# Optimization experiments

Measured on AMD Instinct MI355X. Metric: run time of the kernel, lower is better.

The kernel has to match this reference:

```python
import jax, jax.numpy as jnp
import numpy as np

GAMMA = 1.0
INF_REPLACE = 1e10  # original code replaces inf with 1e10 before logsumexp


def _softmin3(r_diag, r_up, r_left, gamma):
    # softmin over the 3 DP neighbors (stack order matches original: diag, up, left)
    x = jnp.stack([r_diag, r_up, r_left], axis=0)  # (3, B)
    x = jnp.where(jnp.isinf(x), jnp.asarray(INF_REPLACE, x.dtype), x)
    return -gamma * jax.nn.logsumexp(-x / gamma, axis=0)  # (B,)


def _cdist(X, Y):
    # Euclidean pairwise distance, torch.cdist(p=2): (B,N,d),(B,M,d) -> (B,N,M)
    d2 = (jnp.sum(X * X, axis=-1)[:, :, None]
          + jnp.sum(Y * Y, axis=-1)[:, None, :]
          - 2.0 * jnp.einsum('bnd,bmd->bnm', X, Y))
    return jnp.sqrt(jnp.maximum(d2, 0.0))


def _soft_dtw(X, Y, gamma):
    B, N, _ = X.shape
    D = _cdist(X, Y)  # (B, N, N)
    inf = jnp.asarray(jnp.inf, D.dtype)

    # R row 0: [0, inf, inf, ...] per batch
    prev_row0 = jnp.full((B, N + 1), inf, dtype=D.dtype).at[:, 0].set(0.0)

    def row_step(prev_row, d_row):
        # prev_row: (B, N+1) = R[i-1, :]; d_row: (B, N) = D[:, i-1, :]
        xs = (d_row.T, prev_row[:, :-1].T, prev_row[:, 1:].T)  # each (N, B)

        def col_step(r_left, x):
            d, r_diag, r_up = x  # each (B,)
            r = d + _softmin3(r_diag, r_up, r_left, gamma)
            return r, r

        _, row = jax.lax.scan(col_step, jnp.full((B,), inf, dtype=D.dtype), xs)
        new_row = jnp.concatenate([jnp.full((B, 1), inf, dtype=D.dtype), row.T], axis=1)
        return new_row, None

    last_row, _ = jax.lax.scan(row_step, prev_row0, jnp.swapaxes(D, 0, 1))
    return last_row[:, -1]  # R[:, N, N], shape (B,)


def setup_inputs() -> dict:
    key = jax.random.key(0)
    kx, ky = jax.random.split(key)
    B, N, d = 64, 512, 64
    X = jax.random.normal(kx, (B, N, d), dtype=jnp.float32)
    Y = jax.random.normal(ky, (B, N, d), dtype=jnp.float32)
    return {"X": X, "Y": Y}


def reference(X, Y):
    return _soft_dtw(X, Y, GAMMA)
```

## Files before the change

kernel.cpp:

```cpp
#include <hip/hip_runtime.h>
#include <math.h>

#define NB 64
#define NN 512
#define ND 64

#define LOG2E 1.4426950408889634f
#define LN2   0.6931471805599453f
#define RING  12
#define NINF  __int_as_float(0xFF800000u)

typedef __attribute__((ext_vector_type(8))) short  bf16x8;
typedef __attribute__((ext_vector_type(4))) float  f32x4;

static __device__ __forceinline__ unsigned short f2bf(float f) {
    unsigned u = __float_as_uint(f);
    u += 0x7FFFu + ((u >> 16) & 1u);
    return (unsigned short)(u >> 16);
}

__global__ __launch_bounds__(256) void pack_kernel(const float* __restrict__ X,
                                                   const float* __restrict__ Y,
                                                   unsigned short* __restrict__ Xp,
                                                   unsigned short* __restrict__ Yp,
                                                   float* __restrict__ nx,
                                                   float* __restrict__ ny) {
    const int gid = blockIdx.x * 256 + threadIdx.x;
    const float* src;
    unsigned short* dst;
    float* ndst;
    if (blockIdx.y == 0) { src = X + (size_t)gid * ND; dst = Xp; ndst = nx; }
    else                 { src = Y + (size_t)gid * ND; dst = Yp; ndst = ny; }

    float v[ND];
    float s = 0.f;
    #pragma unroll
    for (int k = 0; k < ND; k += 4) {
        float4 f = *(const float4*)(src + k);
        v[k] = f.x; v[k + 1] = f.y; v[k + 2] = f.z; v[k + 3] = f.w;
        s += f.x * f.x + f.y * f.y + f.z * f.z + f.w * f.w;
    }
    ndst[gid] = s;

    const int b  = gid >> 9;
    const int i  = gid & 511;
    const int it = i >> 4;
    const int lm = i & 15;
    #pragma unroll
    for (int h = 0; h < 2; ++h) {
        #pragma unroll
        for (int q = 0; q < 4; ++q) {
            unsigned w[4];
            #pragma unroll
            for (int m = 0; m < 4; ++m) {
                const int c = h * 32 + q * 8 + 2 * m;
                w[m] = (unsigned)f2bf(v[c]) | ((unsigned)f2bf(v[c + 1]) << 16);
            }
            uint4 pkt; pkt.x = w[0]; pkt.y = w[1]; pkt.z = w[2]; pkt.w = w[3];
            *(uint4*)(dst + ((((size_t)b * 32 + it) * 2 + h) << 9)
                          + (size_t)(q * 16 + lm) * 8) = pkt;
        }
    }
}

__global__ __launch_bounds__(256) void cdist_kernel(const unsigned short* __restrict__ Xp,
                                                    const unsigned short* __restrict__ Yp,
                                                    const float* __restrict__ nx,
                                                    const float* __restrict__ ny,
                                                    unsigned short* __restrict__ Wt) {
    const int b  = blockIdx.z;
    const int ib = blockIdx.x * 128;
    const int jb = blockIdx.y * 128;
    const int t  = threadIdx.x;

    const int wave = t >> 6;
    const int wi   = (wave & 1) * 64;
    const int wj   = (wave >> 1) * 64;
    const int lane = t & 63;
    const int lm   = lane & 15;
    const int quad = lane >> 4;

    f32x4 acc[4][4];
    #pragma unroll
    for (int mt = 0; mt < 4; ++mt)
        #pragma unroll
        for (int nt = 0; nt < 4; ++nt)
            acc[mt][nt] = (f32x4){0.f, 0.f, 0.f, 0.f};

    const int jt0 = (jb + wj) >> 4;
    const int it0 = (ib + wi) >> 4;

    #pragma unroll
    for (int h = 0; h < 2; ++h) {
        bf16x8 Af[4], Bf[4];
        #pragma unroll
        for (int mt = 0; mt < 4; ++mt)
            Af[mt] = *(const bf16x8*)(Yp
                + ((((size_t)b * 32 + jt0 + mt) * 2 + h) << 9) + (size_t)lane * 8);
        #pragma unroll
        for (int nt = 0; nt < 4; ++nt)
            Bf[nt] = *(const bf16x8*)(Xp
                + ((((size_t)b * 32 + it0 + nt) * 2 + h) << 9) + (size_t)lane * 8);
        #pragma unroll
        for (int mt = 0; mt < 4; ++mt)
            #pragma unroll
            for (int nt = 0; nt < 4; ++nt)
                acc[mt][nt] = __builtin_amdgcn_mfma_f32_16x16x32_bf16(
                    Af[mt], Bf[nt], acc[mt][nt], 0, 0, 0);
    }

    float nxv[4];
    float4 nyv[4];
    #pragma unroll
    for (int nt = 0; nt < 4; ++nt)
        nxv[nt] = nx[(size_t)b * NN + ib + wi + nt * 16 + lm];
    #pragma unroll
    for (int mt = 0; mt < 4; ++mt)
        nyv[mt] = *(const float4*)(ny + (size_t)b * NN + jb + wj + mt * 16 + quad * 4);

    #pragma unroll
    for (int nt = 0; nt < 4; ++nt) {
        const int i = ib + wi + nt * 16 + lm;
        unsigned short* Drow = Wt + ((size_t)b * NN + i) * NN + jb + wj;
        #pragma unroll
        for (int mt = 0; mt < 4; ++mt) {
            const float* nyp = (const float*)&nyv[mt];
            unsigned a[4];
            #pragma unroll
            for (int r = 0; r < 4; ++r) {
                float d2 = nyp[r] + nxv[nt] - 2.0f * acc[mt][nt][r];
                float w  = __builtin_amdgcn_exp2f(16.0f - LOG2E * sqrtf(fmaxf(d2, 0.f)));
                a[r] = __float_as_uint(w) + 0x8000u;
            }
            uint2 pkt;
            pkt.x = (a[0] >> 16) | (a[1] & 0xFFFF0000u);
            pkt.y = (a[2] >> 16) | (a[3] & 0xFFFF0000u);
            *(uint2*)(Drow + mt * 16 + quad * 4) = pkt;
        }
    }
}

static __device__ __forceinline__ void dtw_step(
    bool DOACT, bool DOGUARD, bool DOREN, bool DOCLAMP,
    int ss, int u, int t, const unsigned short* __restrict__ Wb, int ib,
    uint4* ring, float* L, float& diagHold, float& h, float& Otf)
{
    const float recvH = __int_as_float(__builtin_amdgcn_update_dpp(
        (int)0xFF800000, __float_as_int(h), 0x138 , 0xf, 0xf, false));

    if (DOACT) { if (ss == t && t > 0) Otf = -recvH; }

    const float up0   = __builtin_amdgcn_exp2f(fminf(recvH + Otf, 80.0f));
    const float diag0 = diagHold;
    diagHold = up0 * 65536.0f;

    const int j = ss - t + 1;
    const uint4 c = ring[u];

    {
        int jn = j + RING;
        if (DOCLAMP) jn = jn < 1 ? 1 : jn;
        ring[u] = *(const uint4*)(Wb + (size_t)(jn - 1) * NN + ib);
    }

    bool act = true;
    if (DOGUARD) act = (j >= 1) && (j <= NN);
    if (act) {
        float dd[8];
        dd[0] = __uint_as_float(c.x << 16);
        dd[1] = __uint_as_float(c.x & 0xFFFF0000u);
        dd[2] = __uint_as_float(c.y << 16);
        dd[3] = __uint_as_float(c.y & 0xFFFF0000u);
        dd[4] = __uint_as_float(c.z << 16);
        dd[5] = __uint_as_float(c.z & 0xFFFF0000u);
        dd[6] = __uint_as_float(c.w << 16);
        dd[7] = __uint_as_float(c.w & 0xFFFF0000u);

        float pre[8], cc[8];
        pre[0] = diag0 + L[0];
        #pragma unroll
        for (int k = 1; k < 8; ++k)
            pre[k] = fmaf(65536.0f, L[k - 1], L[k]);
        #pragma unroll
        for (int k = 0; k < 8; ++k) cc[k] = dd[k] * pre[k];
        float r = up0;
        #pragma unroll
        for (int k = 0; k < 8; ++k) {
            r = fmaf(dd[k], r, cc[k]);
            L[k] = r;
        }

        if (DOREN) {
            float m8 = fmaxf(fmaxf(fmaxf(L[0], L[1]), fmaxf(L[2], L[3])),
                             fmaxf(fmaxf(L[4], L[5]), fmaxf(L[6], L[7])));
            const int   e  = (int)(__float_as_uint(m8) >> 23) - 127;
            const float sc = __uint_as_float((unsigned)(127 - e) << 23);
            #pragma unroll
            for (int k = 0; k < 8; ++k) L[k] *= sc;
            diagHold *= sc;
            Otf -= (float)e;
        }

        h = __builtin_amdgcn_logf(L[7]) - Otf;
    }
}

__global__ __launch_bounds__(64) void dtw_kernel(const unsigned short* __restrict__ Wt,
                                                 float* __restrict__ out) {
    const int b = blockIdx.x;
    const int t = threadIdx.x;
    const unsigned short* __restrict__ Wb = Wt + (size_t)b * NN * NN;
    const int ib = 8 * t;

    float L[8];
    #pragma unroll
    for (int k = 0; k < 8; ++k) L[k] = 0.0f;

    float diagHold = (t == 0) ? 65536.0f : 0.0f;
    float h        = NINF;
    float Otf      = 0.0f;

    uint4 ring[RING];
    #pragma unroll
    for (int u = 0; u < RING; ++u) {
        int col = u - t + 1;
        col = col < 1 ? 1 : col;
        ring[u] = *(const uint4*)(Wb + (size_t)(col - 1) * NN + ib);
    }

    for (int sb = 0; sb < 72; sb += RING)
        #pragma unroll
        for (int u = 0; u < RING; ++u)
            dtw_step(true, true, (u & 1) == 1, true,
                     sb + u, u, t, Wb, ib, ring, L, diagHold, h, Otf);

    for (int sb = 72; sb < 504; sb += RING)
        #pragma unroll
        for (int u = 0; u < RING; ++u)
            dtw_step(false, false, (u & 1) == 1, false,
                     sb + u, u, t, Wb, ib, ring, L, diagHold, h, Otf);

    for (int sb = 504; sb < 576; sb += RING)
        #pragma unroll
        for (int u = 0; u < RING; ++u)
            dtw_step(false, true, (u & 1) == 1, false,
                     sb + u, u, t, Wb, ib, ring, L, diagHold, h, Otf);

    if (t == 63) out[b] = (16384.0f - h) * LN2;
}

extern "C" void kernel_launch(void* const* d_in, const int* in_sizes, int n_in,
                              void* d_out, int out_size, void* d_ws, size_t ws_size,
                              hipStream_t stream) {
    const float* X = (const float*)d_in[0];
    const float* Y = (const float*)d_in[1];
    float* out = (float*)d_out;

    char* ws = (char*)d_ws;
    unsigned short* Wt = (unsigned short*)(ws);
    unsigned short* Xp = (unsigned short*)(ws + (33554432));
    unsigned short* Yp = (unsigned short*)(ws + (33554432 + 4194304));
    float* nx = (float*)(ws + (33554432 + 2 * 4194304));
    float* ny = (float*)(ws + (33554432 + 2 * 4194304 + 131072));

    pack_kernel<<<dim3(NB * NN / 256, 2), 256, 0, stream>>>(X, Y, Xp, Yp, nx, ny);
    cdist_kernel<<<dim3(4, 4, NB), 256, 0, stream>>>(Xp, Yp, nx, ny, Wt);
    dtw_kernel<<<NB, 64, 0, stream>>>(Wt, out);
}
```

Baseline: 153.4 us.

## Split soft-DTW wavefront across two waves with LDS handoff of boundary rows

The DTW kernel now uses two 64-lane waves per batch, each owning 256 rows with 4 rows per lane instead of 8, so the serial dependency chain per step is halved. Wave 1 runs two chunks behind wave 0 and receives wave 0's last-row values through shared memory, exchanged once per 64-step chunk with a block barrier and shifted across lanes via DPP. The ring prefetch depth grows to 16 with narrower loads. The cost is roughly 128 extra steps of pipeline fill, eleven block barriers, and LDS traffic, while the number of waves per CU doubles.

New measurement: 147.3 us. 1.04x faster.

```diff
diff --git a/kernel.cpp b/kernel.cpp
--- a/kernel.cpp
+++ b/kernel.cpp
@@ -7,7 +7,7 @@
 
 #define LOG2E 1.4426950408889634f
 #define LN2   0.6931471805599453f
-#define RING  12
+#define RING  16
 #define NINF  __int_as_float(0xFF800000u)
 
 typedef __attribute__((ext_vector_type(8))) short  bf16x8;
@@ -140,113 +140,138 @@
     }
 }
 
-static __device__ __forceinline__ void dtw_step(
-    bool DOACT, bool DOGUARD, bool DOREN, bool DOCLAMP,
+static __device__ __forceinline__ float dpp_shr1(float x, float old) {
+    return __int_as_float(__builtin_amdgcn_update_dpp(
+        __float_as_int(old), __float_as_int(x), 0x138, 0xf, 0xf, false));
+}
+static __device__ __forceinline__ float dpp_shl1(float x) {
+    return __int_as_float(__builtin_amdgcn_update_dpp(
+        0, __float_as_int(x), 0x130, 0xf, 0xf, false));
+}
+
+static __device__ __forceinline__ void dtw_step4(
+    bool W1, bool DOACT, bool DOGUARD, bool DOCLAMP, bool DOREN,
     int ss, int u, int t, const unsigned short* __restrict__ Wb, int ib,
-    uint4* ring, float* L, float& diagHold, float& h, float& Otf)
+    uint2* ring, float* L, float& diagHold, float& h, float& Otf,
+    float& hbuf, float* __restrict__ h0)
 {
-    const float recvH = __int_as_float(__builtin_amdgcn_update_dpp(
-        (int)0xFF800000, __float_as_int(h), 0x138 , 0xf, 0xf, false));
-
-    if (DOACT) { if (ss == t && t > 0) Otf = -recvH; }
+    float recvH = dpp_shr1(h, NINF);
+    if (W1) {
+        recvH = (t == 0) ? hbuf : recvH;
+        hbuf  = dpp_shl1(hbuf);
+    }
+    if (DOACT) { if (ss == t && (t > 0 || W1)) Otf = -recvH; }
 
     const float up0   = __builtin_amdgcn_exp2f(fminf(recvH + Otf, 80.0f));
     const float diag0 = diagHold;
     diagHold = up0 * 65536.0f;
 
     const int j = ss - t + 1;
-    const uint4 c = ring[u];
+    const uint2 c = ring[u];
 
     {
         int jn = j + RING;
         if (DOCLAMP) jn = jn < 1 ? 1 : jn;
-        ring[u] = *(const uint4*)(Wb + (size_t)(jn - 1) * NN + ib);
+        ring[u] = *(const uint2*)(Wb + (size_t)(jn - 1) * NN + ib);
     }
 
     bool act = true;
     if (DOGUARD) act = (j >= 1) && (j <= NN);
     if (act) {
-        float dd[8];
+        float dd[4];
         dd[0] = __uint_as_float(c.x << 16);
         dd[1] = __uint_as_float(c.x & 0xFFFF0000u);
         dd[2] = __uint_as_float(c.y << 16);
         dd[3] = __uint_as_float(c.y & 0xFFFF0000u);
-        dd[4] = __uint_as_float(c.z << 16);
-        dd[5] = __uint_as_float(c.z & 0xFFFF0000u);
-        dd[6] = __uint_as_float(c.w << 16);
-        dd[7] = __uint_as_float(c.w & 0xFFFF0000u);
-
-        float pre[8], cc[8];
+
+        float pre[4], cc[4];
         pre[0] = diag0 + L[0];
         #pragma unroll
-        for (int k = 1; k < 8; ++k)
+        for (int k = 1; k < 4; ++k)
             pre[k] = fmaf(65536.0f, L[k - 1], L[k]);
         #pragma unroll
-        for (int k = 0; k < 8; ++k) cc[k] = dd[k] * pre[k];
+        for (int k = 0; k < 4; ++k) cc[k] = dd[k] * pre[k];
         float r = up0;
         #pragma unroll
-        for (int k = 0; k < 8; ++k) {
+        for (int k = 0; k < 4; ++k) {
             r = fmaf(dd[k], r, cc[k]);
             L[k] = r;
         }
 
         if (DOREN) {
-            float m8 = fmaxf(fmaxf(fmaxf(L[0], L[1]), fmaxf(L[2], L[3])),
-                             fmaxf(fmaxf(L[4], L[5]), fmaxf(L[6], L[7])));
-            const int   e  = (int)(__float_as_uint(m8) >> 23) - 127;
+            float m4 = fmaxf(fmaxf(L[0], L[1]), fmaxf(L[2], L[3]));
+            const int   e  = (int)(__float_as_uint(m4) >> 23) - 127;
             const float sc = __uint_as_float((unsigned)(127 - e) << 23);
             #pragma unroll
-            for (int k = 0; k < 8; ++k) L[k] *= sc;
+            for (int k = 0; k < 4; ++k) L[k] *= sc;
             diagHold *= sc;
             Otf -= (float)e;
         }
 
-        h = __builtin_amdgcn_logf(L[7]) - Otf;
-    }
-}
-
-__global__ __launch_bounds__(64) void dtw_kernel(const unsigned short* __restrict__ Wt,
-                                                 float* __restrict__ out) {
-    const int b = blockIdx.x;
-    const int t = threadIdx.x;
+        h = __builtin_amdgcn_logf(L[3]) - Otf;
+        if (!W1) h0[j] = h;
+    }
+}
+
+static __device__ __forceinline__ void run_chunk(
+    bool W1, bool ACT, bool GUARD, bool CLAMP, int base,
+    int t, const unsigned short* __restrict__ Wb, int ib,
+    uint2* ring, float* L, float& diagHold, float& h, float& Otf,
+    float& hbuf, float* __restrict__ h0)
+{
+    for (int sb = 0; sb < 64; sb += RING)
+        #pragma unroll
+        for (int u = 0; u < RING; ++u)
+            dtw_step4(W1, ACT, GUARD, CLAMP, (u & 1) == 1,
+                      base + sb + u, u, t, Wb, ib, ring, L,
+                      diagHold, h, Otf, hbuf, h0);
+}
+
+__global__ __launch_bounds__(128) void dtw_kernel(const unsigned short* __restrict__ Wt,
+                                                  float* __restrict__ out) {
+    __shared__ float h0[584];
+    const int b    = blockIdx.x;
+    const int tid  = threadIdx.x;
+    const int t    = tid & 63;
+    const int wave = tid >> 6;
     const unsigned short* __restrict__ Wb = Wt + (size_t)b * NN * NN;
-    const int ib = 8 * t;
-
-    float L[8];
-    #pragma unroll
-    for (int k = 0; k < 8; ++k) L[k] = 0.0f;
-
-    float diagHold = (t == 0) ? 65536.0f : 0.0f;
-    float h        = NINF;
-    float Otf      = 0.0f;
-
-    uint4 ring[RING];
+    const int ib = wave * 256 + 4 * t;
+
+    float L[4] = {0.f, 0.f, 0.f, 0.f};
+    float diagHold = (wave == 0 && t == 0) ? 65536.0f : 0.0f;
+    float h = NINF, Otf = 0.0f, hbuf = NINF;
+
+    uint2 ring[RING];
     #pragma unroll
     for (int u = 0; u < RING; ++u) {
         int col = u - t + 1;
         col = col < 1 ? 1 : col;
-        ring[u] = *(const uint4*)(Wb + (size_t)(col - 1) * NN + ib);
-    }
-
-    for (int sb = 0; sb < 72; sb += RING)
-        #pragma unroll
-        for (int u = 0; u < RING; ++u)
-            dtw_step(true, true, (u & 1) == 1, true,
-                     sb + u, u, t, Wb, ib, ring, L, diagHold, h, Otf);
-
-    for (int sb = 72; sb < 504; sb += RING)
-        #pragma unroll
-        for (int u = 0; u < RING; ++u)
-            dtw_step(false, false, (u & 1) == 1, false,
-                     sb + u, u, t, Wb, ib, ring, L, diagHold, h, Otf);
-
-    for (int sb = 504; sb < 576; sb += RING)
-        #pragma unroll
-        for (int u = 0; u < RING; ++u)
-            dtw_step(false, true, (u & 1) == 1, false,
-                     sb + u, u, t, Wb, ib, ring, L, diagHold, h, Otf);
-
-    if (t == 63) out[b] = (16384.0f - h) * LN2;
+        ring[u] = *(const uint2*)(Wb + (size_t)(col - 1) * NN + ib);
+    }
+
+    for (int wall = 0; wall < 11; ++wall) {
+        const int ch = wave ? wall - 2 : wall;
+        if (wave == 0) {
+            if (ch == 0)
+                run_chunk(false, true,  true,  true,  0,      t, Wb, ib, ring, L, diagHold, h, Otf, hbuf, h0);
+            else if (ch >= 1 && ch <= 7)
+                run_chunk(false, false, false, false, ch*64,  t, Wb, ib, ring, L, diagHold, h, Otf, hbuf, h0);
+            else if (ch == 8)
+                run_chunk(false, false, true,  false, 512,    t, Wb, ib, ring, L, diagHold, h, Otf, hbuf, h0);
+        } else {
+            if (ch == 0)
+                run_chunk(true,  true,  true,  true,  0,      t, Wb, ib, ring, L, diagHold, h, Otf, hbuf, h0);
+            else if (ch >= 1 && ch <= 7)
+                run_chunk(true,  false, false, false, ch*64,  t, Wb, ib, ring, L, diagHold, h, Otf, hbuf, h0);
+            else if (ch == 8)
+                run_chunk(true,  false, true,  false, 512,    t, Wb, ib, ring, L, diagHold, h, Otf, hbuf, h0);
+        }
+        __syncthreads();
+        if (wave && wall >= 1 && wall <= 9)
+            hbuf = h0[(wall - 1) * 64 + 1 + t];
+    }
+
+    if (wave == 1 && t == 63) out[b] = (16384.0f - h) * LN2;
 }
 
 extern "C" void kernel_launch(void* const* d_in, const int* in_sizes, int n_in,
@@ -265,5 +290,5 @@
 
     pack_kernel<<<dim3(NB * NN / 256, 2), 256, 0, stream>>>(X, Y, Xp, Yp, nx, ny);
     cdist_kernel<<<dim3(4, 4, NB), 256, 0, stream>>>(Xp, Yp, nx, ny, Wt);
-    dtw_kernel<<<NB, 64, 0, stream>>>(Wt, out);
-}
+    dtw_kernel<<<NB, 128, 0, stream>>>(Wt, out);
+}
```

## Interleave two batch DTW chains per wavefront and pass log as mantissa/exponent

Applied to the files above, without the earlier changes.

Each DTW block now processes two batch items with interleaved independent recurrences, launching half as many blocks, so the latency of one serial chain can be hidden by the other. The log/exp2 pair on the critical path is replaced by passing the neighbor value as a mantissa plus an integer exponent and rebuilding it with integer exponent arithmetic. The prefetch ring shrinks from 12 to 8 entries per chain to limit register pressure. The trade-off is fewer wavefronts across the GPU (32 instead of 64), higher register use per thread, and a shorter prefetch distance.

Measured after the change: 219.4 us. 43.1% more time.

```diff
diff --git a/kernel.cpp b/kernel.cpp
--- a/kernel.cpp
+++ b/kernel.cpp
@@ -7,8 +7,7 @@
 
 #define LOG2E 1.4426950408889634f
 #define LN2   0.6931471805599453f
-#define RING  12
-#define NINF  __int_as_float(0xFF800000u)
+#define RING  8
 
 typedef __attribute__((ext_vector_type(8))) short  bf16x8;
 typedef __attribute__((ext_vector_type(4))) float  f32x4;
@@ -140,19 +139,36 @@
     }
 }
 
-static __device__ __forceinline__ void dtw_step(
-    bool DOACT, bool DOGUARD, bool DOREN, bool DOCLAMP,
+static __device__ __forceinline__ float dpp_shr1f(float x, float old) {
+    return __int_as_float(__builtin_amdgcn_update_dpp(
+        __float_as_int(old), __float_as_int(x), 0x138, 0xf, 0xf, false));
+}
+static __device__ __forceinline__ int dpp_shr1i(int x, int old) {
+    return __builtin_amdgcn_update_dpp(old, x, 0x138, 0xf, 0xf, false);
+}
+
+struct DtwState {
+    float L[8];
+    float diagHold;
+    float hm;
+    int   he;
+    int   Oti;
+};
+
+static __device__ __forceinline__ void half_step(
+    bool DOACT, bool DOGUARD, bool DOCLAMP, bool DOREN,
     int ss, int u, int t, const unsigned short* __restrict__ Wb, int ib,
-    uint4* ring, float* L, float& diagHold, float& h, float& Otf)
+    uint4* ring, DtwState& S)
 {
-    const float recvH = __int_as_float(__builtin_amdgcn_update_dpp(
-        (int)0xFF800000, __float_as_int(h), 0x138 , 0xf, 0xf, false));
-
-    if (DOACT) { if (ss == t && t > 0) Otf = -recvH; }
-
-    const float up0   = __builtin_amdgcn_exp2f(fminf(recvH + Otf, 80.0f));
-    const float diag0 = diagHold;
-    diagHold = up0 * 65536.0f;
+    const float rm = dpp_shr1f(S.hm, 1.0f);
+    const int   re = dpp_shr1i(S.he, -100000);
+    if (DOACT) { if (ss == t && t > 0) S.Oti = -re; }
+
+    int sx = re + S.Oti;
+    sx = sx < -126 ? -126 : (sx > 60 ? 60 : sx);
+    const float up0 = __uint_as_float(__float_as_uint(rm) + ((unsigned)sx << 23));
+    const float diag0 = S.diagHold;
+    S.diagHold = up0 * 65536.0f;
 
     const int j = ss - t + 1;
     const uint4 c = ring[u];
@@ -177,76 +193,87 @@
         dd[7] = __uint_as_float(c.w & 0xFFFF0000u);
 
         float pre[8], cc[8];
-        pre[0] = diag0 + L[0];
+        pre[0] = diag0 + S.L[0];
         #pragma unroll
         for (int k = 1; k < 8; ++k)
-            pre[k] = fmaf(65536.0f, L[k - 1], L[k]);
+            pre[k] = fmaf(65536.0f, S.L[k - 1], S.L[k]);
         #pragma unroll
         for (int k = 0; k < 8; ++k) cc[k] = dd[k] * pre[k];
         float r = up0;
         #pragma unroll
         for (int k = 0; k < 8; ++k) {
             r = fmaf(dd[k], r, cc[k]);
-            L[k] = r;
+            S.L[k] = r;
         }
 
         if (DOREN) {
-            float m8 = fmaxf(fmaxf(fmaxf(L[0], L[1]), fmaxf(L[2], L[3])),
-                             fmaxf(fmaxf(L[4], L[5]), fmaxf(L[6], L[7])));
+            float m8 = fmaxf(fmaxf(fmaxf(S.L[0], S.L[1]), fmaxf(S.L[2], S.L[3])),
+                             fmaxf(fmaxf(S.L[4], S.L[5]), fmaxf(S.L[6], S.L[7])));
             const int   e  = (int)(__float_as_uint(m8) >> 23) - 127;
             const float sc = __uint_as_float((unsigned)(127 - e) << 23);
             #pragma unroll
-            for (int k = 0; k < 8; ++k) L[k] *= sc;
-            diagHold *= sc;
-            Otf -= (float)e;
-        }
-
-        h = __builtin_amdgcn_logf(L[7]) - Otf;
+            for (int k = 0; k < 8; ++k) S.L[k] *= sc;
+            S.diagHold *= sc;
+            S.Oti -= e;
+        }
+
+        const unsigned lb = __float_as_uint(S.L[7]);
+        S.he = (int)(lb >> 23) - 127 - S.Oti;
+        S.hm = __uint_as_float((lb & 0x007FFFFFu) | 0x3F800000u);
     }
 }
 
 __global__ __launch_bounds__(64) void dtw_kernel(const unsigned short* __restrict__ Wt,
                                                  float* __restrict__ out) {
-    const int b = blockIdx.x;
-    const int t = threadIdx.x;
-    const unsigned short* __restrict__ Wb = Wt + (size_t)b * NN * NN;
+    const int bp = blockIdx.x;
+    const int t  = threadIdx.x;
+    const unsigned short* __restrict__ Wb0 = Wt + (size_t)(2 * bp) * NN * NN;
+    const unsigned short* __restrict__ Wb1 = Wt + (size_t)(2 * bp + 1) * NN * NN;
     const int ib = 8 * t;
 
-    float L[8];
-    #pragma unroll
-    for (int k = 0; k < 8; ++k) L[k] = 0.0f;
-
-    float diagHold = (t == 0) ? 65536.0f : 0.0f;
-    float h        = NINF;
-    float Otf      = 0.0f;
-
-    uint4 ring[RING];
+    DtwState S0, S1;
+    #pragma unroll
+    for (int k = 0; k < 8; ++k) { S0.L[k] = 0.f; S1.L[k] = 0.f; }
+    S0.diagHold = (t == 0) ? 65536.0f : 0.0f;
+    S1.diagHold = S0.diagHold;
+    S0.hm = 1.0f; S1.hm = 1.0f;
+    S0.he = -100000; S1.he = -100000;
+    S0.Oti = 0; S1.Oti = 0;
+
+    uint4 ring0[RING], ring1[RING];
     #pragma unroll
     for (int u = 0; u < RING; ++u) {
         int col = u - t + 1;
         col = col < 1 ? 1 : col;
-        ring[u] = *(const uint4*)(Wb + (size_t)(col - 1) * NN + ib);
+        ring0[u] = *(const uint4*)(Wb0 + (size_t)(col - 1) * NN + ib);
+        ring1[u] = *(const uint4*)(Wb1 + (size_t)(col - 1) * NN + ib);
     }
 
     for (int sb = 0; sb < 72; sb += RING)
         #pragma unroll
-        for (int u = 0; u < RING; ++u)
-            dtw_step(true, true, (u & 1) == 1, true,
-                     sb + u, u, t, Wb, ib, ring, L, diagHold, h, Otf);
+        for (int u = 0; u < RING; ++u) {
+            half_step(true, true, true, (u & 1) == 1, sb + u, u, t, Wb0, ib, ring0, S0);
+            half_step(true, true, true, (u & 1) == 1, sb + u, u, t, Wb1, ib, ring1, S1);
+        }
 
     for (int sb = 72; sb < 504; sb += RING)
         #pragma unroll
-        for (int u = 0; u < RING; ++u)
-            dtw_step(false, false, (u & 1) == 1, false,
-                     sb + u, u, t, Wb, ib, ring, L, diagHold, h, Otf);
+        for (int u = 0; u < RING; ++u) {
+            half_step(false, false, false, (u & 1) == 1, sb + u, u, t, Wb0, ib, ring0, S0);
+            half_step(false, false, false, (u & 1) == 1, sb + u, u, t, Wb1, ib, ring1, S1);
+        }
 
     for (int sb = 504; sb < 576; sb += RING)
         #pragma unroll
-        for (int u = 0; u < RING; ++u)
-            dtw_step(false, true, (u & 1) == 1, false,
-                     sb + u, u, t, Wb, ib, ring, L, diagHold, h, Otf);
-
-    if (t == 63) out[b] = (16384.0f - h) * LN2;
+        for (int u = 0; u < RING; ++u) {
+            half_step(false, true, false, (u & 1) == 1, sb + u, u, t, Wb0, ib, ring0, S0);
+            half_step(false, true, false, (u & 1) == 1, sb + u, u, t, Wb1, ib, ring1, S1);
+        }
+
+    if (t == 63) {
+        out[2 * bp]     = (16384.0f - ((float)S0.he + __builtin_amdgcn_logf(S0.hm))) * LN2;
+        out[2 * bp + 1] = (16384.0f - ((float)S1.he + __builtin_amdgcn_logf(S1.hm))) * LN2;
+    }
 }
 
 extern "C" void kernel_launch(void* const* d_in, const int* in_sizes, int n_in,
@@ -265,5 +292,5 @@
 
     pack_kernel<<<dim3(NB * NN / 256, 2), 256, 0, stream>>>(X, Y, Xp, Yp, nx, ny);
     cdist_kernel<<<dim3(4, 4, NB), 256, 0, stream>>>(Xp, Yp, nx, ny, Wt);
-    dtw_kernel<<<NB, 64, 0, stream>>>(Wt, out);
-}
+    dtw_kernel<<<NB / 2, 64, 0, stream>>>(Wt, out);
+}
```
